# Performance work log

Hardware: AMD Instinct MI355X
Metric: run time of the kernel (lower is better)

The kernel has to match this reference:

```python
import jax, jax.numpy as jnp
import numpy as np

N, D = 4096, 512
TAU, ALPHA, EPS = 0.2, 0.5, 1e-15
L2_EPS = 1e-12  # F.normalize eps


def setup_inputs() -> dict:
    key = jax.random.key(0)
    ks = jax.random.split(key, 12)
    # xavier_normal_ with gain=1.414 for [D, D] linears
    std = 1.414 * (2.0 / (D + D)) ** 0.5
    xn = lambda k: jax.random.normal(k, (D, D), jnp.float32) * std
    return {
        "z1": jax.random.normal(ks[0], (N, D), jnp.float32),
        "z2": jax.random.normal(ks[1], (N, D), jnp.float32),
        # local projector: Linear -> PReLU -> Linear
        "lw1": xn(ks[2]), "lb1": jnp.zeros((D,), jnp.float32),
        "la": jnp.full((1,), 0.25, jnp.float32),  # PReLU weight (torch default 0.25)
        "lw2": xn(ks[3]), "lb2": jnp.zeros((D,), jnp.float32),
        # global projector
        "gw1": xn(ks[4]), "gb1": jnp.zeros((D,), jnp.float32),
        "ga": jnp.full((1,), 0.25, jnp.float32),
        "gw2": xn(ks[5]), "gb2": jnp.zeros((D,), jnp.float32),
        # discriminator bilinear weight
        "W": xn(ks[6]),
        # binary positive-pair mask [N, N]
        "mask": jax.random.randint(ks[7], (N, N), 0, 2, jnp.int32),
    }


def _prelu(x, a):
    return jnp.where(x >= 0, x, a * x)


def _proj(z, w1, b1, a, w2, b2):
    # nn.Sequential(Linear, PReLU, Linear); torch Linear: z @ W.T + b
    return _prelu(z @ w1.T + b1, a[0]) @ w2.T + b2


def _l2norm(z):
    n = jnp.linalg.norm(z, axis=-1, keepdims=True)
    return z / jnp.maximum(n, L2_EPS)


def _infonce(h1, h2, m, tau):
    a = _l2norm(h1)
    b = _l2norm(h2)
    sim_intra = jnp.exp(a @ a.T / tau)  # [N, N]
    sim_inter = jnp.exp(a @ b.T / tau)  # [N, N]
    num = (sim_inter * m).sum(1)
    den = sim_intra.sum(1) + sim_inter.sum(1) - (sim_intra * m).sum(1)
    return (-jnp.log(num / den)).mean()


def reference(z1, z2, lw1, lb1, la, lw2, lb2, gw1, gb1, ga, gw2, gb2, W, mask):
    m = mask.astype(jnp.float32)
    # local (node-level) InfoNCE through the local projector
    h1 = _proj(z1, lw1, lb1, la, lw2, lb2)
    h2 = _proj(z2, lw1, lb1, la, lw2, lb2)
    local = 0.5 * (_infonce(h1, h2, m, TAU) + _infonce(h2, h1, m.T, TAU))

    # global (DGI-style) loss
    def gloss(pos_z, neg_z):
        s = pos_z.mean(0)                               # readout [D]
        h = _proj(s, gw1, gb1, ga, gw2, gb2)            # global projector [D]
        summ = W @ h                                    # [D]
        d_pos = jax.nn.sigmoid(pos_z @ summ)            # [N]
        d_neg = jax.nn.sigmoid(neg_z @ summ)            # [N]
        pos_loss = -jnp.log(d_pos + EPS).mean()
        neg_loss = -jnp.log(1.0 - d_neg + EPS).mean()
        return 0.5 * (pos_loss + neg_loss)

    glob = 0.5 * (gloss(z1, z2) + gloss(z2, z1))
    return ALPHA * local + (1.0 - ALPHA) * glob
```

## Files before the change

kernel.cpp:

```cpp
#include <hip/hip_runtime.h>
#include <math.h>

#define NN 4096
#define DD 512
#define INV_TAU 5.0f
#define EPSV 1e-15f

typedef unsigned short u16;
typedef unsigned long long u64;
typedef __attribute__((ext_vector_type(8))) short short8;
typedef __attribute__((ext_vector_type(4))) float f32x4;

__device__ __forceinline__ void gld16(const void* g, void* l) {
  __builtin_amdgcn_global_load_lds(
      (const __attribute__((address_space(1))) unsigned int*)g,
      (__attribute__((address_space(3))) unsigned int*)l, 16, 0, 0);
}

__device__ __forceinline__ void bar_vm2() {
  asm volatile("s_waitcnt vmcnt(2) lgkmcnt(0)\n\ts_barrier" ::: "memory");
}
__device__ __forceinline__ void bar_vm1() {
  asm volatile("s_waitcnt vmcnt(1) lgkmcnt(0)\n\ts_barrier" ::: "memory");
}
__device__ __forceinline__ void bar_vm0() {
  asm volatile("s_waitcnt vmcnt(0) lgkmcnt(0)\n\ts_barrier" ::: "memory");
}

__device__ __forceinline__ float bf2f(u16 u) {
  return __uint_as_float(((unsigned)u) << 16);
}
__device__ __forceinline__ u16 f2bf(float x) {
  unsigned u = __float_as_uint(x);
  u += 0x7fff + ((u >> 16) & 1);
  return (u16)(u >> 16);
}

__device__ __forceinline__ float wave_sum(float v) {
#pragma unroll
  for (int o = 32; o > 0; o >>= 1) v += __shfl_down(v, o, 64);
  return v;
}

__global__ __launch_bounds__(256) void tobf16cm(
    const float* __restrict__ a, const float* __restrict__ b,
    const float* __restrict__ c, const float* __restrict__ d2,
    u16* __restrict__ o, float* __restrict__ pc1, float* __restrict__ pc2,
    float* __restrict__ zbf) {
  const int bid = blockIdx.x, tid = threadIdx.x;
  if (bid >= 4608) {
    const int blk = bid - 4608;
    const int r0 = blk * 32;
    float a0 = 0.f, a1 = 0.f, c0 = 0.f, c1 = 0.f;
    for (int r = r0; r < r0 + 32; ++r) {
      const size_t ro = (size_t)r * DD;
      a0 += c[ro + tid];
      a1 += c[ro + 256 + tid];
      c0 += d2[ro + tid];
      c1 += d2[ro + 256 + tid];
    }
    pc1[blk * 512 + tid] = a0;
    pc1[blk * 512 + 256 + tid] = a1;
    pc2[blk * 512 + tid] = c0;
    pc2[blk * 512 + 256 + tid] = c1;
    return;
  }
  if (bid < 128) zbf[bid * 256 + tid] = 0.f;
  const int i = bid * 256 + tid;
  int j = i;
  const float* s;
  if (j < 65536) {
    s = a + (size_t)j * 4;
  } else {
    j -= 65536;
    if (j < 65536) {
      s = b + (size_t)j * 4;
    } else {
      j -= 65536;
      if (j < 524288) {
        s = c + (size_t)j * 4;
      } else {
        j -= 524288;
        s = d2 + (size_t)j * 4;
      }
    }
  }
  float4 v = *(const float4*)s;
  u64 pk = (u64)f2bf(v.x) | ((u64)f2bf(v.y) << 16) | ((u64)f2bf(v.z) << 32) |
           ((u64)f2bf(v.w) << 48);
  *(u64*)&o[(size_t)i * 4] = pk;
}

template <int ACT>
__global__ __launch_bounds__(512) void gemm_mv(
    const u16* __restrict__ A, const u16* __restrict__ Bw,
    const float* __restrict__ bias, const float* __restrict__ alpha_p,
    u16* __restrict__ out, const float* __restrict__ Mw,
    const float* __restrict__ mx1, const float* __restrict__ mx2,
    const float* __restrict__ mbias, const float* __restrict__ mal,
    float* __restrict__ my1, float* __restrict__ my2) {
  __shared__ __align__(16) u16 sh[3 * 6144];
  __shared__ float svb[512];
  const int tid = threadIdx.x, w = tid >> 6, lane = tid & 63;
  if (blockIdx.x < 64) {
    const int mb = blockIdx.x;
    const int bz = mb >> 5, bx = mb & 31;
    const float* xin = bz ? mx2 : mx1;
    float* y = bz ? my2 : my1;
    if (ACT) {
      float a = 0.f;
      for (int b = 0; b < 128; ++b) a += xin[b * 512 + tid];
      svb[tid] = a * (1.f / NN);
    } else {
      svb[tid] = xin[tid];
    }
    __syncthreads();
#pragma unroll
    for (int rr = 0; rr < 2; ++rr) {
      const int row = bx * 16 + w * 2 + rr;
      float acc = 0.f;
#pragma unroll
      for (int q = 0; q < 8; ++q)
        acc = fmaf(Mw[(size_t)row * DD + lane + 64 * q], svb[lane + 64 * q],
                   acc);
      acc = wave_sum(acc);
      if (lane == 0) {
        acc += mbias[row];
        if (ACT) {
          const float al = mal[0];
          acc = (acc >= 0.f) ? acc : al * acc;
        }
        y[row] = acc;
      }
    }
    return;
  }
  const int quad = lane >> 4, m16 = lane & 15;
  const int wi = w >> 1, wj = w & 1;
  const int bid2 = blockIdx.x - 64;
  const int xcd = bid2 & 7, idx = bid2 >> 3;
  const int i0 = (4 * xcd + (idx & 3)) * 128;
  const int j0 = ((idx >> 2) & 7) * 64;
  const int bz = idx >> 5;
  const u16* Ab = A + (size_t)bz * ((size_t)NN * DD);
  u16* ob = out + (size_t)bz * ((size_t)NN * DD);
  const int roff =
      (m16 >> 1) * 64 + (((((m16 & 1) << 2) | quad) ^ (m16 >> 1)) * 8);
  const int st = (lane & 7) ^ (lane >> 3);
  const int srow = 2 * (lane >> 3) + (st >> 2);
  const int scol = (st & 3) * 8;
  const u16* gs = (w < 4) ? Ab : Bw;
  const int grow0 = ((w < 4) ? i0 + 2 * w * 16 : j0 + (w - 4) * 16) + srow;
  const int doff0 = (w < 4) ? 2 * w * 512 : 4096 + (w - 4) * 512;
  auto stage = [&](int bo, int k) {
    const int kn = k * 32;
    gld16(&gs[(size_t)grow0 * DD + kn + scol], sh + bo + doff0);
    if (w < 4)
      gld16(&gs[(size_t)(grow0 + 16) * DD + kn + scol], sh + bo + doff0 + 512);
  };
  stage(0, 0);
  stage(6144, 1);
  if (w < 4) bar_vm2(); else bar_vm1();
  f32x4 acc[2][2] = {};
  int ro = 0;
  for (int kc = 0; kc < 16; ++kc) {
    if (kc <= 13) {
      int so = ro + 12288;
      if (so >= 18432) so -= 18432;
      stage(so, kc + 2);
    }
    const u16* As = sh + ro;
    const u16* Bs = sh + ro + 4096;
    short8 ar[2], br[2];
#pragma unroll
    for (int s = 0; s < 2; ++s) {
      ar[s] = *(const short8*)&As[(wi * 32 + s * 16) * 32 + roff];
      br[s] = *(const short8*)&Bs[(wj * 32 + s * 16) * 32 + roff];
    }
    __builtin_amdgcn_s_setprio(1);
#pragma unroll
    for (int si = 0; si < 2; ++si)
#pragma unroll
      for (int sj = 0; sj < 2; ++sj)
        acc[si][sj] = __builtin_amdgcn_mfma_f32_16x16x32_bf16(
            ar[si], br[sj], acc[si][sj], 0, 0, 0);
    __builtin_amdgcn_s_setprio(0);
    if (kc <= 13) {
      if (w < 4) bar_vm2(); else bar_vm1();
    } else if (kc == 14) {
      bar_vm0();
    }
    ro += 6144;
    if (ro == 18432) ro = 0;
  }
  const float al = ACT ? alpha_p[0] : 0.f;
#pragma unroll
  for (int si = 0; si < 2; ++si)
#pragma unroll
    for (int sj = 0; sj < 2; ++sj) {
      const int col = j0 + wj * 32 + sj * 16 + m16;
      const float bv = bias[col];
#pragma unroll
      for (int r = 0; r < 4; ++r) {
        const int row = i0 + wi * 32 + si * 16 + quad * 4 + r;
        float x = acc[si][sj][r] + bv;
        if (ACT) x = (x >= 0.f) ? x : al * x;
        ob[(size_t)row * DD + col] = f2bf(x);
      }
    }
}

__global__ __launch_bounds__(256) void rownorm_mv(
    const u16* __restrict__ h, u16* __restrict__ o,
    const float* __restrict__ W, const float* __restrict__ hx1,
    const float* __restrict__ hx2, float* __restrict__ sm1,
    float* __restrict__ sm2) {
  const int bid = blockIdx.x, tid = threadIdx.x;
  const int lane = tid & 63, w = tid >> 6;
  if (bid < 256) {
    const int bz = bid >> 7, bx = bid & 127;
    const float* x = bz ? hx2 : hx1;
    float* y = bz ? sm2 : sm1;
    const int row = bx * 4 + w;
    float acc = 0.f;
#pragma unroll
    for (int q = 0; q < 8; ++q)
      acc = fmaf(W[(size_t)row * DD + lane + 64 * q], x[lane + 64 * q], acc);
    acc = wave_sum(acc);
    if (lane == 0) y[row] = acc;
    return;
  }
  const int row = (bid - 256) * 4 + w;
  const size_t base = (size_t)row * DD + lane * 8;
  short8 v = *(const short8*)&h[base];
  float f[8];
  float s = 0.f;
#pragma unroll
  for (int j = 0; j < 8; ++j) {
    f[j] = bf2f((u16)v[j]);
    s += f[j] * f[j];
  }
  s = wave_sum(s);
  const float inv = 1.f / fmaxf(sqrtf(__shfl(s, 0, 64)), 1e-12f);
  short8 r;
#pragma unroll
  for (int j = 0; j < 8; ++j) r[j] = (short)f2bf(f[j] * inv);
  *(short8*)&o[base] = r;
}

__global__ __launch_bounds__(512, 4) void sim_mfma(
    const u16* __restrict__ na, const u16* __restrict__ nb,
    const int* __restrict__ mask, float* __restrict__ zb,
    const float* __restrict__ z1g, const float* __restrict__ z2g,
    const float* __restrict__ sm1, const float* __restrict__ sm2,
    float* __restrict__ plsP, float* __restrict__ plsN) {
  __shared__ __align__(16) u16 shm[2 * 4 * 4096];
  const int tid = threadIdx.x;
  const int w = tid >> 6, lane = tid & 63;
  if (blockIdx.y < 2) {
    const int lx = blockIdx.y * 32 + blockIdx.x;
    const int bz = lx >> 5, bx5 = lx & 31;
    const float* z = bz ? z2g : z1g;
    const float* sp = bz ? sm2 : sm1;
    const float* sn = bz ? sm1 : sm2;
    float lp = 0.f, ln_ = 0.f;
    for (int k = 0; k < 16; ++k) {
      const int row = bx5 * 128 + w * 16 + k;
      float dp = 0.f, dn = 0.f;
#pragma unroll
      for (int t = 0; t < 8; ++t) {
        const float zv = z[(size_t)row * DD + lane + 64 * t];
        dp = fmaf(zv, sp[lane + 64 * t], dp);
        dn = fmaf(zv, sn[lane + 64 * t], dn);
      }
      dp = wave_sum(dp);
      dn = wave_sum(dn);
      if (lane == 0) {
        lp += -logf(1.f / (1.f + __expf(-dp)) + EPSV);
        ln_ += -logf(1.f - 1.f / (1.f + __expf(-dn)) + EPSV);
      }
    }
    float* red = (float*)shm;
    if (lane == 0) { red[w] = lp; red[8 + w] = ln_; }
    __syncthreads();
    if (tid == 0) {
      float sP = 0.f, sN = 0.f;
      for (int q = 0; q < 8; ++q) { sP += red[q]; sN += red[8 + q]; }
      plsP[lx] = sP;
      plsN[lx] = sN;
    }
    return;
  }
  const int quad = lane >> 4, m16 = lane & 15;
  const int ig = w & 3, jh = w >> 2;
  const int i0 = (blockIdx.y - 2) * 128, j0 = blockIdx.x * 128;
  const int roff =
      (m16 >> 1) * 64 + (((((m16 & 1) << 2) | quad) ^ (m16 >> 1)) * 8);
  const int st = (lane & 7) ^ (lane >> 3);
  const int srow = 2 * (lane >> 3) + (st >> 2);
  const int scol = (st & 3) * 8;
  const int p = w >> 1, rh = (w & 1) * 64;
  const u16* gs = (p & 1) ? nb : na;
  const int gr = ((p < 2) ? i0 : j0) + rh + srow;
  u16* dst0 = shm + p * 4096 + rh * 32;
  auto stage = [&](int bo, int k) {
    const int kn = k * 32;
#pragma unroll
    for (int rr = 0; rr < 64; rr += 16)
      gld16(&gs[(size_t)(gr + rr) * DD + kn + scol], dst0 + bo + rr * 32);
  };
  stage(0, 0);
  bar_vm0();
  f32x4 a11[2][4] = {}, a12[2][4] = {}, a22[2][4] = {};
  int ro = 0;
  for (int kc = 0; kc < 16; ++kc) {
    if (kc < 15) stage(ro ^ 16384, kc + 1);
    const u16* Ai = shm + ro;
    const u16* Bi = shm + ro + 4096;
    const u16* Aj = shm + ro + 8192;
    const u16* Bj = shm + ro + 12288;
    short8 ai0 = *(const short8*)&Ai[(ig * 32) * 32 + roff];
    short8 ai1 = *(const short8*)&Ai[(ig * 32 + 16) * 32 + roff];
    short8 bi0 = *(const short8*)&Bi[(ig * 32) * 32 + roff];
    short8 bi1 = *(const short8*)&Bi[(ig * 32 + 16) * 32 + roff];
#pragma unroll
    for (int c = 0; c < 4; ++c) {
      short8 aj = *(const short8*)&Aj[(jh * 64 + c * 16) * 32 + roff];
      short8 bj = *(const short8*)&Bj[(jh * 64 + c * 16) * 32 + roff];
      __builtin_amdgcn_s_setprio(1);
      a11[0][c] = __builtin_amdgcn_mfma_f32_16x16x32_bf16(ai0, aj, a11[0][c], 0, 0, 0);
      a11[1][c] = __builtin_amdgcn_mfma_f32_16x16x32_bf16(ai1, aj, a11[1][c], 0, 0, 0);
      a12[0][c] = __builtin_amdgcn_mfma_f32_16x16x32_bf16(ai0, bj, a12[0][c], 0, 0, 0);
      a12[1][c] = __builtin_amdgcn_mfma_f32_16x16x32_bf16(ai1, bj, a12[1][c], 0, 0, 0);
      a22[0][c] = __builtin_amdgcn_mfma_f32_16x16x32_bf16(bi0, bj, a22[0][c], 0, 0, 0);
      a22[1][c] = __builtin_amdgcn_mfma_f32_16x16x32_bf16(bi1, bj, a22[1][c], 0, 0, 0);
      __builtin_amdgcn_s_setprio(0);
    }
    if (kc < 15) {
      bar_vm0();
      ro ^= 16384;
    }
  }
  float* rred = (float*)shm;
  float* cred = rred + 512;
  rred[tid] = 0.f;
  rred[tid + 512] = 0.f;
  __syncthreads();
  float rs11[2][4] = {}, rm11[2][4] = {}, rs12[2][4] = {}, rm12[2][4] = {};
  float cs12[4] = {}, cm12[4] = {}, cs22[4] = {}, cm22[4] = {};
#pragma unroll
  for (int t = 0; t < 2; ++t) {
    int mreg[4][4];
#pragma unroll
    for (int r = 0; r < 4; ++r) {
      const int gi = i0 + ig * 32 + t * 16 + quad * 4 + r;
      const int* mrow = &mask[(size_t)gi * NN + j0 + jh * 64];
#pragma unroll
      for (int c = 0; c < 4; ++c) mreg[r][c] = mrow[c * 16 + m16];
    }
#pragma unroll
    for (int c = 0; c < 4; ++c) {
#pragma unroll
      for (int r = 0; r < 4; ++r) {
        const float mv = (float)mreg[r][c];
        const float e11 = __expf(a11[t][c][r] * INV_TAU);
        const float e12 = __expf(a12[t][c][r] * INV_TAU);
        const float e22 = __expf(a22[t][c][r] * INV_TAU);
        rs11[t][r] += e11;
        rm11[t][r] += e11 * mv;
        rs12[t][r] += e12;
        rm12[t][r] += e12 * mv;
        cs12[c] += e12;
        cm12[c] += e12 * mv;
        cs22[c] += e22;
        cm22[c] += e22 * mv;
      }
    }
  }
#pragma unroll
  for (int t = 0; t < 2; ++t)
#pragma unroll
    for (int r = 0; r < 4; ++r) {
      float v0 = rs11[t][r], v1 = rm11[t][r], v2 = rs12[t][r], v3 = rm12[t][r];
#pragma unroll
      for (int o = 1; o < 16; o <<= 1) {
        v0 += __shfl_xor(v0, o, 64);
        v1 += __shfl_xor(v1, o, 64);
        v2 += __shfl_xor(v2, o, 64);
        v3 += __shfl_xor(v3, o, 64);
      }
      if (m16 == 0) {
        const int il = ig * 32 + t * 16 + quad * 4 + r;
        atomicAdd(&rred[0 * 128 + il], v0);
        atomicAdd(&rred[1 * 128 + il], v1);
        atomicAdd(&rred[2 * 128 + il], v2);
        atomicAdd(&rred[3 * 128 + il], v3);
      }
    }
#pragma unroll
  for (int c = 0; c < 4; ++c) {
    float v0 = cs12[c], v1 = cm12[c], v2 = cs22[c], v3 = cm22[c];
    v0 += __shfl_xor(v0, 16, 64); v0 += __shfl_xor(v0, 32, 64);
    v1 += __shfl_xor(v1, 16, 64); v1 += __shfl_xor(v1, 32, 64);
    v2 += __shfl_xor(v2, 16, 64); v2 += __shfl_xor(v2, 32, 64);
    v3 += __shfl_xor(v3, 16, 64); v3 += __shfl_xor(v3, 32, 64);
    if (lane < 16) {
      const int jl = jh * 64 + c * 16 + lane;
      atomicAdd(&cred[0 * 128 + jl], v0);
      atomicAdd(&cred[1 * 128 + jl], v1);
      atomicAdd(&cred[2 * 128 + jl], v2);
      atomicAdd(&cred[3 * 128 + jl], v3);
    }
  }
  __syncthreads();
  if (tid < 128) {
#pragma unroll
    for (int q = 0; q < 4; ++q)
      atomicAdd(&zb[q * NN + i0 + tid], rred[q * 128 + tid]);
  } else if (tid < 256) {
    const int jl = tid - 128;
#pragma unroll
    for (int q = 0; q < 4; ++q)
      atomicAdd(&zb[(4 + q) * NN + j0 + jl], cred[q * 128 + jl]);
  }
}

__global__ __launch_bounds__(512) void fin(const float* __restrict__ zb,
                                           const float* __restrict__ plsP,
                                           const float* __restrict__ plsN,
                                           float* __restrict__ out) {
  const int tid = threadIdx.x;
  const int lane = tid & 63, w = tid >> 6;
  float S1 = 0.f, S2 = 0.f;
#pragma unroll
  for (int k = 0; k < 8; ++k) {
    const int i = tid + k * 512;
    const float r11 = zb[i], r11m = zb[NN + i];
    const float r12 = zb[2 * NN + i], r12m = zb[3 * NN + i];
    const float c12 = zb[4 * NN + i], c12m = zb[5 * NN + i];
    const float c22 = zb[6 * NN + i], c22m = zb[7 * NN + i];
    S1 += -logf(r12m / (r11 + r12 - r11m));
    S2 += -logf(c12m / (c22 + c12 - c22m));
  }
  float G = (tid < 64) ? (plsP[tid] + plsN[tid]) : 0.f;
  S1 = wave_sum(S1);
  S2 = wave_sum(S2);
  G = wave_sum(G);
  __shared__ float fr[3][8];
  if (lane == 0) { fr[0][w] = S1; fr[1][w] = S2; fr[2][w] = G; }
  __syncthreads();
  if (tid == 0) {
    float s1t = 0.f, s2t = 0.f, gt = 0.f;
    for (int q = 0; q < 8; ++q) {
      s1t += fr[0][q];
      s2t += fr[1][q];
      gt += fr[2][q];
    }
    const float local = 0.5f * (s1t + s2t) * (1.f / NN);
    const float glob = 0.25f * gt * (1.f / NN);
    out[0] = 0.5f * local + 0.5f * glob;
  }
}

extern "C" void kernel_launch(void* const* d_in, const int* in_sizes, int n_in,
                              void* d_out, int out_size, void* d_ws,
                              size_t ws_size, hipStream_t stream) {
  const float* z1 = (const float*)d_in[0];
  const float* z2 = (const float*)d_in[1];
  const float* lw1 = (const float*)d_in[2];
  const float* lb1 = (const float*)d_in[3];
  const float* la = (const float*)d_in[4];
  const float* lw2 = (const float*)d_in[5];
  const float* lb2 = (const float*)d_in[6];
  const float* gw1 = (const float*)d_in[7];
  const float* gb1 = (const float*)d_in[8];
  const float* ga = (const float*)d_in[9];
  const float* gw2 = (const float*)d_in[10];
  const float* gb2 = (const float*)d_in[11];
  const float* W = (const float*)d_in[12];
  const int* mask = (const int*)d_in[13];
  float* out = (float*)d_out;

  const size_t ND = (size_t)NN * DD;
  u16* W1b = (u16*)d_ws;
  u16* W2b = W1b + 512 * 512;
  u16* Ab = W1b + 2 * 512 * 512;
  u16* Bb = Ab + 2 * ND;
  float* zbf = (float*)(Bb + 2 * ND);
  float* pc1 = zbf + 8 * NN;
  float* pc2 = pc1 + 128 * 512;
  float* t1 = pc2 + 128 * 512;
  float* t2 = t1 + 512;
  float* hg1 = t2 + 512;
  float* hg2 = hg1 + 512;
  float* summ1 = hg2 + 512;
  float* summ2 = summ1 + 512;
  float* plsP = summ2 + 512;
  float* plsN = plsP + 64;

  tobf16cm<<<4736, dim3(256), 0, stream>>>(lw1, lw2, z1, z2, W1b, pc1, pc2,
                                           zbf);
  gemm_mv<1><<<576, dim3(512), 0, stream>>>(Ab, W1b, lb1, la, Bb, gw1, pc1,
                                            pc2, gb1, ga, t1, t2);
  gemm_mv<0><<<576, dim3(512), 0, stream>>>(Bb, W2b, lb2, la, Ab, gw2, t1, t2,
                                            gb2, nullptr, hg1, hg2);
  rownorm_mv<<<2304, dim3(256), 0, stream>>>(Ab, Bb, W, hg1, hg2, summ1,
                                             summ2);
  sim_mfma<<<dim3(32, 34), dim3(512), 0, stream>>>(
      Bb, Bb + ND, mask, zbf, z1, z2, summ1, summ2, plsP, plsN);
  fin<<<1, dim3(512), 0, stream>>>(zbf, plsP, plsN, out);
}
```

Measured before the change: 288.6 us.

## Prefetch mask tile into LDS asynchronously during the MFMA k-loop

The 128x128 int mask tile for each sim block is now streamed into LDS with global_load_lds during the first 8 k-iterations of the MFMA loop, instead of being read from global memory in the epilogue. This hides the mask load latency behind matrix compute. In exchange LDS use per block rises to 128 KB of dynamic shared memory and the occupancy hint is dropped, so at most one 512-thread block fits per CU.

Result: faster. 260.7 us (-9.6%).

```diff
diff --git a/kernel.cpp b/kernel.cpp
--- a/kernel.cpp
+++ b/kernel.cpp
@@ -248,13 +248,13 @@
   *(short8*)&o[base] = r;
 }
 
-__global__ __launch_bounds__(512, 4) void sim_mfma(
+__global__ __launch_bounds__(512) void sim_mfma(
     const u16* __restrict__ na, const u16* __restrict__ nb,
     const int* __restrict__ mask, float* __restrict__ zb,
     const float* __restrict__ z1g, const float* __restrict__ z2g,
     const float* __restrict__ sm1, const float* __restrict__ sm2,
     float* __restrict__ plsP, float* __restrict__ plsN) {
-  __shared__ __align__(16) u16 shm[2 * 4 * 4096];
+  extern __shared__ __align__(16) u16 shm[];
   const int tid = threadIdx.x;
   const int w = tid >> 6, lane = tid & 63;
   if (blockIdx.y < 2) {
@@ -309,12 +309,21 @@
     for (int rr = 0; rr < 64; rr += 16)
       gld16(&gs[(size_t)(gr + rr) * DD + kn + scol], dst0 + bo + rr * 32);
   };
+  char* mldsb = (char*)(shm + 32768);
+  const char* mbase = (const char*)mask + (size_t)i0 * (NN * 4) + (size_t)j0 * 4;
+  const int mrow_l = lane >> 5;
+  const int mcolb = (lane & 31) * 16;
   stage(0, 0);
   bar_vm0();
   f32x4 a11[2][4] = {}, a12[2][4] = {}, a22[2][4] = {};
   int ro = 0;
   for (int kc = 0; kc < 16; ++kc) {
     if (kc < 15) stage(ro ^ 16384, kc + 1);
+    if (kc < 8) {
+      const int ci = kc * 8 + w;
+      gld16(mbase + (size_t)(2 * ci + mrow_l) * (NN * 4) + mcolb,
+            mldsb + ci * 1024);
+    }
     const u16* Ai = shm + ro;
     const u16* Bi = shm + ro + 4096;
     const u16* Aj = shm + ro + 8192;
@@ -343,26 +352,20 @@
   }
   float* rred = (float*)shm;
   float* cred = rred + 512;
+  const int* mint = (const int*)mldsb;
   rred[tid] = 0.f;
   rred[tid + 512] = 0.f;
   __syncthreads();
   float rs11[2][4] = {}, rm11[2][4] = {}, rs12[2][4] = {}, rm12[2][4] = {};
   float cs12[4] = {}, cm12[4] = {}, cs22[4] = {}, cm22[4] = {};
 #pragma unroll
-  for (int t = 0; t < 2; ++t) {
-    int mreg[4][4];
+  for (int t = 0; t < 2; ++t)
 #pragma unroll
     for (int r = 0; r < 4; ++r) {
-      const int gi = i0 + ig * 32 + t * 16 + quad * 4 + r;
-      const int* mrow = &mask[(size_t)gi * NN + j0 + jh * 64];
-#pragma unroll
-      for (int c = 0; c < 4; ++c) mreg[r][c] = mrow[c * 16 + m16];
-    }
-#pragma unroll
-    for (int c = 0; c < 4; ++c) {
-#pragma unroll
-      for (int r = 0; r < 4; ++r) {
-        const float mv = (float)mreg[r][c];
+      const int rloc = ig * 32 + t * 16 + quad * 4 + r;
+#pragma unroll
+      for (int c = 0; c < 4; ++c) {
+        const float mv = (float)mint[rloc * 128 + jh * 64 + c * 16 + m16];
         const float e11 = __expf(a11[t][c][r] * INV_TAU);
         const float e12 = __expf(a12[t][c][r] * INV_TAU);
         const float e22 = __expf(a22[t][c][r] * INV_TAU);
@@ -376,7 +379,6 @@
         cm22[c] += e22 * mv;
       }
     }
-  }
 #pragma unroll
   for (int t = 0; t < 2; ++t)
 #pragma unroll
@@ -481,6 +483,14 @@
   const int* mask = (const int*)d_in[13];
   float* out = (float*)d_out;
 
+  static bool attr_set = false;
+  if (!attr_set) {
+    (void)hipFuncSetAttribute(reinterpret_cast<const void*>(sim_mfma),
+                              hipFuncAttributeMaxDynamicSharedMemorySize,
+                              131072);
+    attr_set = true;
+  }
+
   const size_t ND = (size_t)NN * DD;
   u16* W1b = (u16*)d_ws;
   u16* W2b = W1b + 512 * 512;
@@ -506,7 +516,7 @@
                                             gb2, nullptr, hg1, hg2);
   rownorm_mv<<<2304, dim3(256), 0, stream>>>(Ab, Bb, W, hg1, hg2, summ1,
                                              summ2);
-  sim_mfma<<<dim3(32, 34), dim3(512), 0, stream>>>(
+  sim_mfma<<<dim3(32, 34), dim3(512), 131072, stream>>>(
       Bb, Bb + ND, mask, zbf, z1, z2, summ1, summ2, plsP, plsN);
   fin<<<1, dim3(512), 0, stream>>>(zbf, plsP, plsN, out);
 }
```
